# Performance work log

Hardware: AMD Instinct MI355X
Metric: run time of the kernel (lower is better)

The kernel has to match this reference:

```python
import jax, jax.numpy as jnp
import numpy as np

B, S, D, H, DFF = 4, 2048, 1024, 16, 4096
DK = D // H
EPS = 1e-9


def setup_inputs() -> dict:
    key = jax.random.key(0)
    ks = jax.random.split(key, 12)
    s = lambda k, shape, scale: jax.random.normal(k, shape, dtype=jnp.float32) * scale
    return {
        "x": s(ks[0], (B, S, D), 1.0),
        "mask": jnp.ones((B, 1, 1, S), dtype=jnp.int32),
        # Linear weights stored torch-style [out, in]
        "wq": s(ks[1], (D, D), D ** -0.5),
        "wk": s(ks[2], (D, D), D ** -0.5),
        "wv": s(ks[3], (D, D), D ** -0.5),
        "wo": s(ks[4], (D, D), D ** -0.5),
        "w1": s(ks[5], (DFF, D), D ** -0.5),
        "b1": jnp.zeros((DFF,), jnp.float32),
        "w2": s(ks[6], (D, DFF), DFF ** -0.5),
        "b2": jnp.zeros((D,), jnp.float32),
        "g1": jnp.ones((D,), jnp.float32),
        "be1": jnp.zeros((D,), jnp.float32),
        "g2": jnp.ones((D,), jnp.float32),
        "be2": jnp.zeros((D,), jnp.float32),
    }


def _layernorm(x, gamma, beta):
    # Matches AddAndNorm: torch.std uses Bessel correction (ddof=1)
    mean = jnp.mean(x, axis=-1, keepdims=True)
    var = jnp.sum((x - mean) ** 2, axis=-1, keepdims=True) / (x.shape[-1] - 1)
    return gamma * (x - mean) / jnp.sqrt(var + EPS) + beta


def _mha(x, mask, wq, wk, wv, wo):
    b, s, d = x.shape
    def proj(w):  # [b,s,d] @ [d,d]^T -> heads [b,h,s,dk]
        return (x @ w.T).reshape(b, s, H, DK).transpose(0, 2, 1, 3)
    q, k, v = proj(wq), proj(wk), proj(wv)
    scores = jnp.einsum("bhqd,bhkd->bhqk", q, k) / jnp.sqrt(jnp.float32(DK))
    scores = jnp.where(mask == 0, jnp.float32(-1e9), scores)
    attn = jax.nn.softmax(scores, axis=-1)
    out = jnp.einsum("bhqk,bhkd->bhqd", attn, v)
    out = out.transpose(0, 2, 1, 3).reshape(b, s, d)
    return out @ wo.T


def reference(x, mask, wq, wk, wv, wo, w1, b1, w2, b2, g1, be1, g2, be2):
    # Residual 1: x + MHA(LN(x))  (dropout = 0)
    h1 = x + _mha(_layernorm(x, g1, be1), mask, wq, wk, wv, wo)
    # Residual 2: h1 + FFN(LN(h1))
    z = _layernorm(h1, g2, be2)
    ffn = jax.nn.relu(z @ w1.T + b1) @ w2.T + b2
    return h1 + ffn
```

## Files before the change

kernel.cpp:

```cpp
#include <hip/hip_runtime.h>
#include <hip/hip_bf16.h>
#include <cstdint>
#include <cstddef>

typedef __attribute__((ext_vector_type(8))) short short8;
typedef __attribute__((ext_vector_type(4))) float floatx4;
typedef __attribute__((ext_vector_type(4))) unsigned short ushort4e;

#define B_   4
#define S_   2048
#define D_   1024
#define H_   16
#define DK_  64
#define DFF_ 4096
#define MTOT (B_ * S_)
#define QKVLD 3072

__device__ __forceinline__ float bf2f(unsigned short u) {
    union { unsigned int i; float f; } v; v.i = ((unsigned int)u) << 16; return v.f;
}
__device__ __forceinline__ unsigned short f2bf(float f) {
    union { float f; unsigned int i; } v; v.f = f;
    unsigned int u = v.i;
    u += 0x7fffu + ((u >> 16) & 1u);
    return (unsigned short)(u >> 16);
}
__device__ __forceinline__ void async_cp16(const void* g, void* l) {
    __builtin_amdgcn_global_load_lds(
        (const __attribute__((address_space(1))) unsigned int*)g,
        (__attribute__((address_space(3))) unsigned int*)l,
        16, 0, 0);
}

__global__ void dtype_probe(const unsigned short* __restrict__ x, int* flag) {
    __shared__ float red[4];
    const int tid = threadIdx.x;
    float mx = 0.f;
    #pragma unroll
    for (int i = 0; i < 16; i++) {
        float v = fabsf(bf2f(x[tid * 16 + i]));
        if (v != v) v = 1e30f;
        mx = fmaxf(mx, v);
    }
    #pragma unroll
    for (int off = 32; off > 0; off >>= 1) mx = fmaxf(mx, __shfl_down(mx, off));
    if ((tid & 63) == 0) red[tid >> 6] = mx;
    __syncthreads();
    if (tid == 0) {
        float m = fmaxf(fmaxf(red[0], red[1]), fmaxf(red[2], red[3]));
        *flag = (m > 50.f) ? 1 : 0;
    }
}

__device__ __forceinline__ void cvt8(const void* src, unsigned short* dst, int i, int fl) {
    if (fl) {
        const floatx4* s = (const floatx4*)src;
        floatx4 a = s[i * 2], b = s[i * 2 + 1];
        short8 o;
        o[0] = (short)f2bf(a[0]); o[1] = (short)f2bf(a[1]);
        o[2] = (short)f2bf(a[2]); o[3] = (short)f2bf(a[3]);
        o[4] = (short)f2bf(b[0]); o[5] = (short)f2bf(b[1]);
        o[6] = (short)f2bf(b[2]); o[7] = (short)f2bf(b[3]);
        ((short8*)dst)[i] = o;
    } else {
        ((short8*)dst)[i] = ((const short8*)src)[i];
    }
}

__global__ void cvt_kernel(const void* __restrict__ src,
                           unsigned short* __restrict__ dst,
                           int n8, const int* __restrict__ flag) {
    const int i = blockIdx.x * 256 + threadIdx.x;
    if (i >= n8) return;
    cvt8(src, dst, i, *flag);
}

__global__ void cvt4_kernel(const void* s0, const void* s1, const void* s2, const void* s3,
                            unsigned short* __restrict__ dst,
                            const int* __restrict__ flag) {
    const int t = blockIdx.x >> 9;
    const int i = (blockIdx.x & 511) * 256 + threadIdx.x;
    const void* s = (t == 0) ? s0 : (t == 1) ? s1 : (t == 2) ? s2 : s3;
    cvt8(s, dst + (size_t)t * (D_ * D_), i, *flag);
}

__global__ void cvt_small(const void* b1, const void* b2, const void* g1,
                          const void* be1, const void* g2, const void* be2,
                          unsigned short* db1, unsigned short* db2, unsigned short* dg1,
                          unsigned short* dbe1, unsigned short* dg2, unsigned short* dbe2,
                          const int* __restrict__ flag) {
    const int fl = *flag;
    for (int i = threadIdx.x; i < 1152; i += 256) {
        if (i < 512)       cvt8(b1,  db1,  i,        fl);
        else if (i < 640)  cvt8(b2,  db2,  i - 512,  fl);
        else if (i < 768)  cvt8(g1,  dg1,  i - 640,  fl);
        else if (i < 896)  cvt8(be1, dbe1, i - 768,  fl);
        else if (i < 1024) cvt8(g2,  dg2,  i - 896,  fl);
        else               cvt8(be2, dbe2, i - 1024, fl);
    }
}

#define BM 128
#define BN 128
#define BK 64

template<int RELU, int HAS_BIAS, int RES_MODE, int OUT_MODE>
__global__ __launch_bounds__(256)
void gemm_bt(const unsigned short* __restrict__ A, int lda,
             const unsigned short* __restrict__ W, int ldw,
             const unsigned short* __restrict__ bias,
             const void* resid,
             void* out,
             int M, int N, int K,
             const int* __restrict__ flagp)
{
    __shared__ unsigned short As[BM * BK];
    __shared__ unsigned short Bs[BN * BK];

    const int tid  = threadIdx.x;
    const int lane = tid & 63;
    const int wave = tid >> 6;
    const int wm = wave >> 1;
    const int wn = wave & 1;
    const int lr = lane & 15;
    const int lq = lane >> 4;

    const int m0 = blockIdx.y * BM;
    const int n0 = blockIdx.x * BN;

    int fl = 1;
    if (RES_MODE == 3 || OUT_MODE == 2) fl = *flagp;

    floatx4 acc[4][4];
    #pragma unroll
    for (int i = 0; i < 4; i++)
        #pragma unroll
        for (int j = 0; j < 4; j++)
            acc[i][j] = (floatx4){0.f, 0.f, 0.f, 0.f};

    const int lrow = lane >> 3;
    const int swz  = ((lane & 7) ^ lrow) * 8;
    const int rx   = lr & 7;
    const int p0   = ((lq)     ^ rx) * 8;
    const int p1   = ((4 + lq) ^ rx) * 8;

    for (int k0 = 0; k0 < K; k0 += BK) {
        #pragma unroll
        for (int t = 0; t < 4; t++) {
            const int row = wave * 32 + t * 8;
            async_cp16(A + (size_t)(m0 + row + lrow) * lda + k0 + swz, &As[row * BK]);
            async_cp16(W + (size_t)(n0 + row + lrow) * ldw + k0 + swz, &Bs[row * BK]);
        }
        __syncthreads();
        #pragma unroll
        for (int kk = 0; kk < 2; kk++) {
            const int pos = kk ? p1 : p0;
            short8 af[4], bfr[4];
            #pragma unroll
            for (int i = 0; i < 4; i++) {
                af[i]  = *(const short8*)(&As[(wm * 64 + i * 16 + lr) * BK + pos]);
                bfr[i] = *(const short8*)(&Bs[(wn * 64 + i * 16 + lr) * BK + pos]);
            }
            #pragma unroll
            for (int i = 0; i < 4; i++)
                #pragma unroll
                for (int j = 0; j < 4; j++)
                    acc[i][j] = __builtin_amdgcn_mfma_f32_16x16x32_bf16(
                                    af[i], bfr[j], acc[i][j], 0, 0, 0);
        }
        __syncthreads();
    }

    #pragma unroll
    for (int i = 0; i < 4; i++) {
        #pragma unroll
        for (int j = 0; j < 4; j++) {
            const int col = n0 + wn * 64 + j * 16 + lr;
            const float bv = HAS_BIAS ? bf2f(bias[col]) : 0.f;
            #pragma unroll
            for (int r = 0; r < 4; r++) {
                const int row = m0 + wm * 64 + i * 16 + lq * 4 + r;
                const size_t idx = (size_t)row * N + col;
                float vvv = acc[i][j][r] + bv;
                if (RES_MODE == 1) vvv += bf2f(((const unsigned short*)resid)[idx]);
                if (RES_MODE == 2) vvv += ((const float*)resid)[idx];
                if (RES_MODE == 3) vvv += fl ? ((const float*)resid)[idx]
                                             : bf2f(((const unsigned short*)resid)[idx]);
                if (RELU) vvv = fmaxf(vvv, 0.f);
                if (OUT_MODE == 1)      ((float*)out)[idx] = vvv;
                else if (OUT_MODE == 0) ((unsigned short*)out)[idx] = f2bf(vvv);
                else { if (fl) ((float*)out)[idx] = vvv;
                       else    ((unsigned short*)out)[idx] = f2bf(vvv); }
            }
        }
    }
}

#define GBM 256
#define GBN 256
#define GBK 64

__device__ __forceinline__ void gbar() {
    asm volatile("" ::: "memory");
    __builtin_amdgcn_s_barrier();
    asm volatile("" ::: "memory");
}

template<int RELU, int HAS_BIAS>
__global__ __launch_bounds__(512, 2)
void gemm256_bt(const unsigned short* __restrict__ A, int lda,
                const unsigned short* __restrict__ W, int ldw,
                const unsigned short* __restrict__ bias,
                unsigned short* __restrict__ out,
                int M, int N, int K)
{
    __shared__ unsigned short As[2][GBM * GBK];
    __shared__ unsigned short Bs[2][GBN * GBK];

    const int tid  = threadIdx.x;
    const int lane = tid & 63;
    const int wave = tid >> 6;
    const int wm   = wave >> 2;
    const int wn   = wave & 3;
    const int lr   = lane & 15;
    const int lq   = lane >> 4;

    const int m0 = blockIdx.y * GBM;
    const int n0 = blockIdx.x * GBN;

    const int lrow = lane >> 3;
    const int schk = ((lane & 7) ^ lrow) * 8;
    const int rx   = lr & 7;
    const int fp0  = ((lq)     ^ rx) * 8;
    const int fp1  = ((4 + lq) ^ rx) * 8;

    floatx4 acc[8][4];
    #pragma unroll
    for (int i = 0; i < 8; i++)
        #pragma unroll
        for (int j = 0; j < 4; j++)
            acc[i][j] = (floatx4){0.f, 0.f, 0.f, 0.f};

    const int nkt = K / GBK;

    #pragma unroll
    for (int g = 0; g < 4; g++) {
        async_cp16(A + (size_t)(m0 + g * 64 + wave * 8 + lrow) * lda + schk,
                   &As[0][g * 4096 + wave * 512]);
        async_cp16(W + (size_t)(n0 + g * 64 + wave * 8 + lrow) * ldw + schk,
                   &Bs[0][g * 4096 + wave * 512]);
    }
    asm volatile("s_waitcnt vmcnt(0)" ::: "memory");
    __syncthreads();

    for (int t = 0; t < nkt; ++t) {
        const int cur   = t & 1;
        const int knext = (t + 1) * GBK;
        const bool more = (t + 1 < nkt);
        short8 bfr[4][2];

        #pragma unroll
        for (int p = 0; p < 4; ++p) {
            short8 af[2][2];
            #pragma unroll
            for (int ii = 0; ii < 2; ii++)
                #pragma unroll
                for (int kk = 0; kk < 2; kk++)
                    af[ii][kk] = *(const short8*)
                        &As[cur][(wm * 128 + p * 32 + ii * 16 + lr) * GBK + (kk ? fp1 : fp0)];
            if (p == 0) {
                #pragma unroll
                for (int j = 0; j < 4; j++)
                    #pragma unroll
                    for (int kk = 0; kk < 2; kk++)
                        bfr[j][kk] = *(const short8*)
                            &Bs[cur][(wn * 64 + j * 16 + lr) * GBK + (kk ? fp1 : fp0)];
                if (more) {
                    #pragma unroll
                    for (int g = 0; g < 4; g++)
                        async_cp16(A + (size_t)(m0 + g * 64 + wave * 8 + lrow) * lda + knext + schk,
                                   &As[cur ^ 1][g * 4096 + wave * 512]);
                }
            }
            if (p == 1 && more) {
                #pragma unroll
                for (int g = 0; g < 4; g++)
                    async_cp16(W + (size_t)(n0 + g * 64 + wave * 8 + lrow) * ldw + knext + schk,
                               &Bs[cur ^ 1][g * 4096 + wave * 512]);
            }
            if (p == 3) asm volatile("s_waitcnt vmcnt(0)" ::: "memory");
            gbar();
            __builtin_amdgcn_s_setprio(1);
            #pragma unroll
            for (int kk = 0; kk < 2; kk++)
                #pragma unroll
                for (int ii = 0; ii < 2; ii++)
                    #pragma unroll
                    for (int j = 0; j < 4; j++)
                        acc[p * 2 + ii][j] = __builtin_amdgcn_mfma_f32_16x16x32_bf16(
                                                 af[ii][kk], bfr[j][kk],
                                                 acc[p * 2 + ii][j], 0, 0, 0);
            __builtin_amdgcn_s_setprio(0);
            gbar();
        }
    }

    #pragma unroll
    for (int i = 0; i < 8; i++) {
        #pragma unroll
        for (int j = 0; j < 4; j++) {
            const int col = n0 + wn * 64 + j * 16 + lr;
            const float bv = HAS_BIAS ? bf2f(bias[col]) : 0.f;
            #pragma unroll
            for (int r = 0; r < 4; r++) {
                const int row = m0 + wm * 128 + i * 16 + lq * 4 + r;
                float vvv = acc[i][j][r] + bv;
                if (RELU) vvv = fmaxf(vvv, 0.f);
                out[(size_t)row * N + col] = f2bf(vvv);
            }
        }
    }
}

template<int IN_MODE>
__global__ __launch_bounds__(256)
void ln_kernel(const void* __restrict__ Xv,
               const unsigned short* __restrict__ g,
               const unsigned short* __restrict__ be,
               unsigned short* __restrict__ out,
               const int* __restrict__ flagp)
{
    const int row = blockIdx.x;
    const int tid = threadIdx.x;
    int fl = 1;
    if (IN_MODE == 2) fl = *flagp;
    float x4[4];
    if (IN_MODE == 1 || fl) {
        const float* X = (const float*)Xv + (size_t)row * D_ + tid * 4;
        floatx4 t = *(const floatx4*)X;
        x4[0] = t[0]; x4[1] = t[1]; x4[2] = t[2]; x4[3] = t[3];
    } else {
        const unsigned short* X = (const unsigned short*)Xv + (size_t)row * D_ + tid * 4;
        ushort4e u = *(const ushort4e*)X;
        #pragma unroll
        for (int i = 0; i < 4; i++) x4[i] = bf2f(u[i]);
    }
    float s1 = x4[0] + x4[1] + x4[2] + x4[3];
    float s2 = x4[0]*x4[0] + x4[1]*x4[1] + x4[2]*x4[2] + x4[3]*x4[3];
    #pragma unroll
    for (int off = 32; off > 0; off >>= 1) {
        s1 += __shfl_down(s1, off);
        s2 += __shfl_down(s2, off);
    }
    __shared__ float r1[4], r2[4];
    const int wv = tid >> 6;
    if ((tid & 63) == 0) { r1[wv] = s1; r2[wv] = s2; }
    __syncthreads();
    s1 = r1[0] + r1[1] + r1[2] + r1[3];
    s2 = r2[0] + r2[1] + r2[2] + r2[3];
    const float mean = s1 * (1.0f / D_);
    const float var  = (s2 - (float)D_ * mean * mean) * (1.0f / (D_ - 1));
    const float rstd = rsqrtf(var + 1e-9f);

    ushort4e o4;
    #pragma unroll
    for (int i = 0; i < 4; i++) {
        const float gv = bf2f(g[tid * 4 + i]);
        const float bv = bf2f(be[tid * 4 + i]);
        o4[i] = f2bf(gv * (x4[i] - mean) * rstd + bv);
    }
    *(ushort4e*)(out + (size_t)row * D_ + tid * 4) = o4;
}

__global__ __launch_bounds__(256)
void vtrans(const unsigned short* __restrict__ V, int ldv,
            unsigned short* __restrict__ Vt)
{
    __shared__ unsigned short t[64 * 72];
    const int tid = threadIdx.x;
    const int kt  = blockIdx.x * 64;
    const int bh  = blockIdx.y;
    const int b   = bh >> 4, h = bh & 15;
    const int r   = tid >> 2;
    const int c4  = (tid & 3) * 16;
    const unsigned short* vp = V + (size_t)(b * S_ + kt + r) * ldv + h * DK_ + c4;
    *(short8*)&t[r * 72 + c4]     = *(const short8*)vp;
    *(short8*)&t[r * 72 + c4 + 8] = *(const short8*)(vp + 8);
    __syncthreads();
    short8 o0, o1;
    #pragma unroll
    for (int e = 0; e < 8; e++) {
        o0[e] = (short)t[(c4 + e) * 72 + r];
        o1[e] = (short)t[(c4 + 8 + e) * 72 + r];
    }
    unsigned short* op = Vt + ((size_t)bh * DK_ + r) * S_ + kt + c4;
    *(short8*)op       = o0;
    *(short8*)(op + 8) = o1;
}

#define ATK   64
#define KS_LD 64
#define PS_LD 72
#define NT_   (S_ / ATK)

__global__ __launch_bounds__(256)
void attn_mfma(const unsigned short* __restrict__ QKV,
               const unsigned short* __restrict__ Vt,
               const int* __restrict__ mask,
               unsigned short* __restrict__ ctx)
{
    __shared__ unsigned short Ks[ATK * KS_LD];
    __shared__ unsigned short Vts[DK_ * KS_LD];
    __shared__ unsigned short Ps[4][32 * PS_LD];
    __shared__ float maskadd[ATK];
    __shared__ float ared[4][32];

    const int tid  = threadIdx.x;
    const int lane = tid & 63;
    const int w    = tid >> 6;
    const int c    = lane & 15;
    const int qd   = lane >> 4;

    const int flat    = blockIdx.y * gridDim.x + blockIdx.x;
    const int logical = (flat & 7) * 128 + (flat >> 3);
    const int bh   = logical >> 4;
    const int b    = bh >> 4;
    const int h    = bh & 15;
    const int q0   = (logical & 15) * 128 + w * 32;

    const int lrow = lane >> 3;
    const int swz  = ((lane & 7) ^ lrow) * 8;
    const int cx   = c & 7;

    const float QS = 0.18033688f;
    short8 qf[2][2];
    #pragma unroll
    for (int jq = 0; jq < 2; jq++)
        #pragma unroll
        for (int kk = 0; kk < 2; kk++) {
            const unsigned short* qp =
                QKV + (size_t)(b * S_ + q0 + jq * 16 + c) * QKVLD + h * DK_ + kk * 32 + qd * 8;
            short8 t = *(const short8*)qp;
            short8 o;
            #pragma unroll
            for (int e = 0; e < 8; e++)
                o[e] = (short)f2bf(bf2f((unsigned short)t[e]) * QS);
            qf[jq][kk] = o;
        }

    floatx4 acc_o[2][4];
    #pragma unroll
    for (int iq = 0; iq < 2; iq++)
        #pragma unroll
        for (int jd = 0; jd < 4; jd++)
            acc_o[iq][jd] = (floatx4){0.f, 0.f, 0.f, 0.f};
    float lrun[2] = {0.f, 0.f};

    for (int kt = 0; kt < S_; kt += ATK) {
        {
            const unsigned short* kbase =
                QKV + 1024 + (size_t)(b * S_ + kt + w * 16) * QKVLD + h * DK_;
            const unsigned short* vbase =
                Vt + ((size_t)bh * DK_ + w * 16) * S_ + kt;
            #pragma unroll
            for (int t = 0; t < 2; t++) {
                async_cp16(kbase + (size_t)(t * 8 + lrow) * QKVLD + swz,
                           &Ks[(w * 16 + t * 8) * KS_LD]);
                async_cp16(vbase + (size_t)(t * 8 + lrow) * S_ + swz,
                           &Vts[(w * 16 + t * 8) * KS_LD]);
            }
            if (tid < ATK) maskadd[tid] = (mask[b * S_ + kt + tid] == 0) ? -1e9f : 0.f;
        }
        __syncthreads();

        floatx4 acc_s[4][2];
        #pragma unroll
        for (int i = 0; i < 4; i++)
            #pragma unroll
            for (int jq = 0; jq < 2; jq++)
                acc_s[i][jq] = (floatx4){0.f, 0.f, 0.f, 0.f};
        #pragma unroll
        for (int kk = 0; kk < 2; kk++) {
            const int pos = ((kk * 4 + qd) ^ cx) * 8;
            short8 kf[4];
            #pragma unroll
            for (int i = 0; i < 4; i++)
                kf[i] = *(const short8*)&Ks[(i * 16 + c) * KS_LD + pos];
            __builtin_amdgcn_s_setprio(1);
            #pragma unroll
            for (int i = 0; i < 4; i++)
                #pragma unroll
                for (int jq = 0; jq < 2; jq++)
                    acc_s[i][jq] = __builtin_amdgcn_mfma_f32_16x16x32_bf16(
                                       kf[i], qf[jq][kk], acc_s[i][jq], 0, 0, 0);
            __builtin_amdgcn_s_setprio(0);
        }

        floatx4 madd[4];
        #pragma unroll
        for (int i = 0; i < 4; i++)
            madd[i] = *(const floatx4*)&maskadd[i * 16 + qd * 4];

        #pragma unroll
        for (int jq = 0; jq < 2; jq++) {
            float ps = 0.f;
            #pragma unroll
            for (int i = 0; i < 4; i++) {
                floatx4 p;
                #pragma unroll
                for (int r = 0; r < 4; r++) {
                    p[r] = __builtin_amdgcn_exp2f(acc_s[i][jq][r] + madd[i][r]);
                    ps += p[r];
                }
                unsigned int w0, w1;
                asm("v_cvt_pk_bf16_f32 %0, %1, %2" : "=v"(w0) : "v"(p[0]), "v"(p[1]));
                asm("v_cvt_pk_bf16_f32 %0, %1, %2" : "=v"(w1) : "v"(p[2]), "v"(p[3]));
                uint2 pk; pk.x = w0; pk.y = w1;
                *(uint2*)&Ps[w][(jq * 16 + c) * PS_LD + i * 16 + qd * 4] = pk;
            }
            ps += __shfl_xor(ps, 16);
            ps += __shfl_xor(ps, 32);
            lrun[jq] += ps;
        }

        #pragma unroll
        for (int kk = 0; kk < 2; kk++) {
            const int pos = ((kk * 4 + qd) ^ cx) * 8;
            short8 pf[2], vf[4];
            #pragma unroll
            for (int iq = 0; iq < 2; iq++)
                pf[iq] = *(const short8*)&Ps[w][(iq * 16 + c) * PS_LD + kk * 32 + qd * 8];
            #pragma unroll
            for (int jd = 0; jd < 4; jd++)
                vf[jd] = *(const short8*)&Vts[(jd * 16 + c) * KS_LD + pos];
            __builtin_amdgcn_s_setprio(1);
            #pragma unroll
            for (int iq = 0; iq < 2; iq++)
                #pragma unroll
                for (int jd = 0; jd < 4; jd++)
                    acc_o[iq][jd] = __builtin_amdgcn_mfma_f32_16x16x32_bf16(
                                        pf[iq], vf[jd], acc_o[iq][jd], 0, 0, 0);
            __builtin_amdgcn_s_setprio(0);
        }
        __syncthreads();
    }

    if (lane < 16) { ared[w][c] = 1.f / lrun[0]; ared[w][16 + c] = 1.f / lrun[1]; }
    floatx4 lv0 = *(const floatx4*)&ared[w][qd * 4];
    floatx4 lv1 = *(const floatx4*)&ared[w][16 + qd * 4];
    #pragma unroll
    for (int iq = 0; iq < 2; iq++)
        #pragma unroll
        for (int jd = 0; jd < 4; jd++)
            #pragma unroll
            for (int r = 0; r < 4; r++) {
                const int row = q0 + iq * 16 + qd * 4 + r;
                const int col = h * DK_ + jd * 16 + c;
                const float inv = (iq == 0) ? lv0[r] : lv1[r];
                ctx[(size_t)(b * S_ + row) * D_ + col] = f2bf(acc_o[iq][jd][r] * inv);
            }
}

extern "C" void kernel_launch(void* const* d_in, const int* in_sizes, int n_in,
                              void* d_out, int out_size, void* d_ws, size_t ws_size,
                              hipStream_t stream)
{
    const void* x_raw  = d_in[0];
    const int*  mask   = (const int*)d_in[1];
    const void* wq_raw = d_in[2];
    const void* wk_raw = d_in[3];
    const void* wv_raw = d_in[4];
    const void* wo_raw = d_in[5];
    const void* w1_raw = d_in[6];
    const void* b1_raw = d_in[7];
    const void* w2_raw = d_in[8];
    const void* b2_raw = d_in[9];
    const void* g1_raw = d_in[10];
    const void* be1_raw= d_in[11];
    const void* g2_raw = d_in[12];
    const void* be2_raw= d_in[13];

    char* ws = (char*)d_ws;
    const size_t MB = 1024 * 1024;
    int* flag = (int*)ws;
    unsigned short* cb1  = (unsigned short*)(ws + 1 * 1024);
    unsigned short* cb2  = (unsigned short*)(ws + 16 * 1024);
    unsigned short* cg1  = (unsigned short*)(ws + 32 * 1024);
    unsigned short* cbe1 = (unsigned short*)(ws + 40 * 1024);
    unsigned short* cg2  = (unsigned short*)(ws + 48 * 1024);
    unsigned short* cbe2 = (unsigned short*)(ws + 56 * 1024);
    unsigned short* cwqkvo = (unsigned short*)(ws + 1 * MB);
    unsigned short* cwqkv  = cwqkvo;
    unsigned short* cwo    = cwqkvo + 3 * (D_ * D_);
    unsigned short* cw1  = (unsigned short*)(ws + 9 * MB);
    unsigned short* cw2  = (unsigned short*)(ws + 17 * MB);
    unsigned short* xn1  = (unsigned short*)(ws + 25 * MB);
    unsigned short* ctx  = (unsigned short*)(ws + 25 * MB);
    unsigned short* zbuf = (unsigned short*)(ws + 25 * MB);
    unsigned short* qkv  = (unsigned short*)(ws + 41 * MB);
    float*          h1   = (float*)(ws + 57 * MB);
    unsigned short* vt   = (unsigned short*)d_out;
    unsigned short* xn2  = (unsigned short*)d_out;

    dtype_probe<<<1, 256, 0, stream>>>((const unsigned short*)x_raw, flag);
    cvt_small<<<1, 256, 0, stream>>>(b1_raw, b2_raw, g1_raw, be1_raw, g2_raw, be2_raw,
                                     cb1, cb2, cg1, cbe1, cg2, cbe2, flag);
    cvt4_kernel<<<2048, 256, 0, stream>>>(wq_raw, wk_raw, wv_raw, wo_raw, cwqkvo, flag);
    cvt_kernel<<<(DFF_ * D_ / 8 + 255) / 256, 256, 0, stream>>>(w1_raw, cw1, DFF_ * D_ / 8, flag);
    cvt_kernel<<<(D_ * DFF_ / 8 + 255) / 256, 256, 0, stream>>>(w2_raw, cw2, D_ * DFF_ / 8, flag);

    const dim3 blk(256);
    const dim3 blk5(512);
    const dim3 gs(D_ / BN, MTOT / BM);
    const dim3 gq256(QKVLD / GBN, MTOT / GBM);
    const dim3 gf256(2048 / GBN, MTOT / GBM);

    ln_kernel<2><<<MTOT, blk, 0, stream>>>(x_raw, cg1, cbe1, xn1, flag);
    gemm256_bt<0,0><<<gq256, blk5, 0, stream>>>(xn1, D_, cwqkv, D_, nullptr, qkv, MTOT, QKVLD, D_);
    vtrans<<<dim3(S_ / 64, B_ * H_), blk, 0, stream>>>(qkv + 2048, QKVLD, vt);
    attn_mfma<<<dim3(S_ / 128, B_ * H_), blk, 0, stream>>>(qkv, vt, mask, ctx);
    gemm_bt<0,0,3,1><<<gs, blk, 0, stream>>>(ctx, D_, cwo, D_, nullptr, x_raw, h1, MTOT, D_, D_, flag);
    ln_kernel<1><<<MTOT, blk, 0, stream>>>(h1, cg2, cbe2, xn2, flag);
    gemm256_bt<1,1><<<gf256, blk5, 0, stream>>>(xn2, D_, cw1, D_, cb1, zbuf, MTOT, 2048, D_);
    gemm_bt<0,0,2,1><<<gs, blk, 0, stream>>>(zbuf, 2048, cw2, DFF_, nullptr, h1, h1, MTOT, D_, 2048, flag);
    const unsigned short* w1c = cw1 + (size_t)2048 * D_;
    gemm256_bt<1,1><<<gf256, blk5, 0, stream>>>(xn2, D_, w1c, D_, cb1 + 2048, zbuf, MTOT, 2048, D_);
    gemm_bt<0,1,2,2><<<gs, blk, 0, stream>>>(zbuf, 2048, cw2 + 2048, DFF_, cb2, h1, d_out, MTOT, D_, 2048, flag);
}
```

Before: 569.6 us.

## Double attention query rows per block and add XCD-aware tile remapping to GEMMs

```diff
diff --git a/kernel.cpp b/kernel.cpp
--- a/kernel.cpp
+++ b/kernel.cpp
@@ -125,8 +125,11 @@
     const int lr = lane & 15;
     const int lq = lane >> 4;
 
-    const int m0 = blockIdx.y * BM;
-    const int n0 = blockIdx.x * BN;
+    const int nwg     = gridDim.x * gridDim.y;
+    const int flat    = blockIdx.y * gridDim.x + blockIdx.x;
+    const int logical = (flat & 7) * (nwg >> 3) + (flat >> 3);
+    const int m0 = (logical / gridDim.x) * BM;
+    const int n0 = (logical % gridDim.x) * BN;
 
     int fl = 1;
     if (RES_MODE == 3 || OUT_MODE == 2) fl = *flagp;
@@ -225,8 +228,11 @@
     const int lr   = lane & 15;
     const int lq   = lane >> 4;
 
-    const int m0 = blockIdx.y * GBM;
-    const int n0 = blockIdx.x * GBN;
+    const int nwg     = gridDim.x * gridDim.y;
+    const int flat    = blockIdx.y * gridDim.x + blockIdx.x;
+    const int logical = (flat & 7) * (nwg >> 3) + (flat >> 3);
+    const int m0 = (logical / gridDim.x) * GBM;
+    const int n0 = (logical % gridDim.x) * GBN;
 
     const int lrow = lane >> 3;
     const int schk = ((lane & 7) ^ lrow) * 8;
@@ -413,7 +419,7 @@
     __shared__ unsigned short Vts[DK_ * KS_LD];
     __shared__ unsigned short Ps[4][32 * PS_LD];
     __shared__ float maskadd[ATK];
-    __shared__ float ared[4][32];
+    __shared__ float ared[4][64];
 
     const int tid  = threadIdx.x;
     const int lane = tid & 63;
@@ -422,39 +428,44 @@
     const int qd   = lane >> 4;
 
     const int flat    = blockIdx.y * gridDim.x + blockIdx.x;
-    const int logical = (flat & 7) * 128 + (flat >> 3);
-    const int bh   = logical >> 4;
+    const int logical = (flat & 7) * 64 + (flat >> 3);
+    const int bh   = logical >> 3;
     const int b    = bh >> 4;
     const int h    = bh & 15;
-    const int q0   = (logical & 15) * 128 + w * 32;
+    const int qb   = (logical & 7) * 256 + w * 32;
 
     const int lrow = lane >> 3;
     const int swz  = ((lane & 7) ^ lrow) * 8;
     const int cx   = c & 7;
 
     const float QS = 0.18033688f;
-    short8 qf[2][2];
-    #pragma unroll
-    for (int jq = 0; jq < 2; jq++)
-        #pragma unroll
-        for (int kk = 0; kk < 2; kk++) {
-            const unsigned short* qp =
-                QKV + (size_t)(b * S_ + q0 + jq * 16 + c) * QKVLD + h * DK_ + kk * 32 + qd * 8;
-            short8 t = *(const short8*)qp;
-            short8 o;
-            #pragma unroll
-            for (int e = 0; e < 8; e++)
-                o[e] = (short)f2bf(bf2f((unsigned short)t[e]) * QS);
-            qf[jq][kk] = o;
-        }
-
-    floatx4 acc_o[2][4];
-    #pragma unroll
-    for (int iq = 0; iq < 2; iq++)
-        #pragma unroll
-        for (int jd = 0; jd < 4; jd++)
-            acc_o[iq][jd] = (floatx4){0.f, 0.f, 0.f, 0.f};
-    float lrun[2] = {0.f, 0.f};
+    short8 qf[2][2][2];
+    #pragma unroll
+    for (int qh = 0; qh < 2; qh++)
+        #pragma unroll
+        for (int jq = 0; jq < 2; jq++)
+            #pragma unroll
+            for (int kk = 0; kk < 2; kk++) {
+                const unsigned short* qp =
+                    QKV + (size_t)(b * S_ + qb + qh * 128 + jq * 16 + c) * QKVLD
+                        + h * DK_ + kk * 32 + qd * 8;
+                short8 t = *(const short8*)qp;
+                short8 o;
+                #pragma unroll
+                for (int e = 0; e < 8; e++)
+                    o[e] = (short)f2bf(bf2f((unsigned short)t[e]) * QS);
+                qf[qh][jq][kk] = o;
+            }
+
+    floatx4 acc_o[2][2][4];
+    #pragma unroll
+    for (int qh = 0; qh < 2; qh++)
+        #pragma unroll
+        for (int iq = 0; iq < 2; iq++)
+            #pragma unroll
+            for (int jd = 0; jd < 4; jd++)
+                acc_o[qh][iq][jd] = (floatx4){0.f, 0.f, 0.f, 0.f};
+    float lrun[2][2] = {{0.f, 0.f}, {0.f, 0.f}};
 
     for (int kt = 0; kt < S_; kt += ATK) {
         {
@@ -473,92 +484,106 @@
         }
         __syncthreads();
 
-        floatx4 acc_s[4][2];
-        #pragma unroll
-        for (int i = 0; i < 4; i++)
-            #pragma unroll
-            for (int jq = 0; jq < 2; jq++)
-                acc_s[i][jq] = (floatx4){0.f, 0.f, 0.f, 0.f};
-        #pragma unroll
-        for (int kk = 0; kk < 2; kk++) {
-            const int pos = ((kk * 4 + qd) ^ cx) * 8;
-            short8 kf[4];
+        #pragma unroll
+        for (int qh = 0; qh < 2; qh++) {
+            floatx4 acc_s[4][2];
             #pragma unroll
             for (int i = 0; i < 4; i++)
-                kf[i] = *(const short8*)&Ks[(i * 16 + c) * KS_LD + pos];
-            __builtin_amdgcn_s_setprio(1);
+                #pragma unroll
+                for (int jq = 0; jq < 2; jq++)
+                    acc_s[i][jq] = (floatx4){0.f, 0.f, 0.f, 0.f};
+            #pragma unroll
+            for (int kk = 0; kk < 2; kk++) {
+                const int pos = ((kk * 4 + qd) ^ cx) * 8;
+                short8 kf[4];
+                #pragma unroll
+                for (int i = 0; i < 4; i++)
+                    kf[i] = *(const short8*)&Ks[(i * 16 + c) * KS_LD + pos];
+                __builtin_amdgcn_s_setprio(1);
+                #pragma unroll
+                for (int i = 0; i < 4; i++)
+                    #pragma unroll
+                    for (int jq = 0; jq < 2; jq++)
+                        acc_s[i][jq] = __builtin_amdgcn_mfma_f32_16x16x32_bf16(
+                                           kf[i], qf[qh][jq][kk], acc_s[i][jq], 0, 0, 0);
+                __builtin_amdgcn_s_setprio(0);
+            }
+
+            floatx4 madd[4];
             #pragma unroll
             for (int i = 0; i < 4; i++)
-                #pragma unroll
-                for (int jq = 0; jq < 2; jq++)
-                    acc_s[i][jq] = __builtin_amdgcn_mfma_f32_16x16x32_bf16(
-                                       kf[i], qf[jq][kk], acc_s[i][jq], 0, 0, 0);
-            __builtin_amdgcn_s_setprio(0);
-        }
-
-        floatx4 madd[4];
-        #pragma unroll
-        for (int i = 0; i < 4; i++)
-            madd[i] = *(const floatx4*)&maskadd[i * 16 + qd * 4];
-
-        #pragma unroll
-        for (int jq = 0; jq < 2; jq++) {
-            float ps = 0.f;
-            #pragma unroll
-            for (int i = 0; i < 4; i++) {
-                floatx4 p;
-                #pragma unroll
-                for (int r = 0; r < 4; r++) {
-                    p[r] = __builtin_amdgcn_exp2f(acc_s[i][jq][r] + madd[i][r]);
-                    ps += p[r];
+                madd[i] = *(const floatx4*)&maskadd[i * 16 + qd * 4];
+
+            #pragma unroll
+            for (int jq = 0; jq < 2; jq++) {
+                float ps = 0.f;
+                #pragma unroll
+                for (int i = 0; i < 4; i++) {
+                    floatx4 p;
+                    #pragma unroll
+                    for (int r = 0; r < 4; r++) {
+                        p[r] = __builtin_amdgcn_exp2f(acc_s[i][jq][r] + madd[i][r]);
+                        ps += p[r];
+                    }
+                    unsigned int w0, w1;
+                    asm("v_cvt_pk_bf16_f32 %0, %1, %2" : "=v"(w0) : "v"(p[0]), "v"(p[1]));
+                    asm("v_cvt_pk_bf16_f32 %0, %1, %2" : "=v"(w1) : "v"(p[2]), "v"(p[3]));
+                    uint2 pk; pk.x = w0; pk.y = w1;
+                    *(uint2*)&Ps[w][(jq * 16 + c) * PS_LD + i * 16 + qd * 4] = pk;
                 }
-                unsigned int w0, w1;
-                asm("v_cvt_pk_bf16_f32 %0, %1, %2" : "=v"(w0) : "v"(p[0]), "v"(p[1]));
-                asm("v_cvt_pk_bf16_f32 %0, %1, %2" : "=v"(w1) : "v"(p[2]), "v"(p[3]));
-                uint2 pk; pk.x = w0; pk.y = w1;
-                *(uint2*)&Ps[w][(jq * 16 + c) * PS_LD + i * 16 + qd * 4] = pk;
-            }
-            ps += __shfl_xor(ps, 16);
-            ps += __shfl_xor(ps, 32);
-            lrun[jq] += ps;
-        }
-
-        #pragma unroll
-        for (int kk = 0; kk < 2; kk++) {
-            const int pos = ((kk * 4 + qd) ^ cx) * 8;
-            short8 pf[2], vf[4];
-            #pragma unroll
-            for (int iq = 0; iq < 2; iq++)
-                pf[iq] = *(const short8*)&Ps[w][(iq * 16 + c) * PS_LD + kk * 32 + qd * 8];
-            #pragma unroll
-            for (int jd = 0; jd < 4; jd++)
-                vf[jd] = *(const short8*)&Vts[(jd * 16 + c) * KS_LD + pos];
-            __builtin_amdgcn_s_setprio(1);
-            #pragma unroll
-            for (int iq = 0; iq < 2; iq++)
+                ps += __shfl_xor(ps, 16);
+                ps += __shfl_xor(ps, 32);
+                lrun[qh][jq] += ps;
+            }
+
+            #pragma unroll
+            for (int kk = 0; kk < 2; kk++) {
+                const int pos = ((kk * 4 + qd) ^ cx) * 8;
+                short8 pf[2], vf[4];
+                #pragma unroll
+                for (int iq = 0; iq < 2; iq++)
+                    pf[iq] = *(const short8*)&Ps[w][(iq * 16 + c) * PS_LD + kk * 32 + qd * 8];
                 #pragma unroll
                 for (int jd = 0; jd < 4; jd++)
-                    acc_o[iq][jd] = __builtin_amdgcn_mfma_f32_16x16x32_bf16(
-                                        pf[iq], vf[jd], acc_o[iq][jd], 0, 0, 0);
-            __builtin_amdgcn_s_setprio(0);
+                    vf[jd] = *(const short8*)&Vts[(jd * 16 + c) * KS_LD + pos];
+                __builtin_amdgcn_s_setprio(1);
+                #pragma unroll
+                for (int iq = 0; iq < 2; iq++)
+                    #pragma unroll
+                    for (int jd = 0; jd < 4; jd++)
+                        acc_o[qh][iq][jd] = __builtin_amdgcn_mfma_f32_16x16x32_bf16(
+                                                pf[iq], vf[jd], acc_o[qh][iq][jd], 0, 0, 0);
+                __builtin_amdgcn_s_setprio(0);
+            }
         }
         __syncthreads();
     }
 
-    if (lane < 16) { ared[w][c] = 1.f / lrun[0]; ared[w][16 + c] = 1.f / lrun[1]; }
-    floatx4 lv0 = *(const floatx4*)&ared[w][qd * 4];
-    floatx4 lv1 = *(const floatx4*)&ared[w][16 + qd * 4];
-    #pragma unroll
-    for (int iq = 0; iq < 2; iq++)
-        #pragma unroll
-        for (int jd = 0; jd < 4; jd++)
-            #pragma unroll
-            for (int r = 0; r < 4; r++) {
-                const int row = q0 + iq * 16 + qd * 4 + r;
-                const int col = h * DK_ + jd * 16 + c;
-                const float inv = (iq == 0) ? lv0[r] : lv1[r];
-                ctx[(size_t)(b * S_ + row) * D_ + col] = f2bf(acc_o[iq][jd][r] * inv);
-            }
+    if (lane < 16) {
+        ared[w][c]      = 1.f / lrun[0][0];
+        ared[w][16 + c] = 1.f / lrun[0][1];
+        ared[w][32 + c] = 1.f / lrun[1][0];
+        ared[w][48 + c] = 1.f / lrun[1][1];
+    }
+    floatx4 lv[2][2];
+    #pragma unroll
+    for (int qh = 0; qh < 2; qh++)
+        #pragma unroll
+        for (int iq = 0; iq < 2; iq++)
+            lv[qh][iq] = *(const floatx4*)&ared[w][qh * 32 + iq * 16 + qd * 4];
+    #pragma unroll
+    for (int qh = 0; qh < 2; qh++)
+        #pragma unroll
+        for (int iq = 0; iq < 2; iq++)
+            #pragma unroll
+            for (int jd = 0; jd < 4; jd++)
+                #pragma unroll
+                for (int r = 0; r < 4; r++) {
+                    const int row = qb + qh * 128 + iq * 16 + qd * 4 + r;
+                    const int col = h * DK_ + jd * 16 + c;
+                    ctx[(size_t)(b * S_ + row) * D_ + col] =
+                        f2bf(acc_o[qh][iq][jd][r] * lv[qh][iq][r]);
+                }
 }
 
 extern "C" void kernel_launch(void* const* d_in, const int* in_sizes, int n_in,
@@ -618,7 +643,7 @@
     ln_kernel<2><<<MTOT, blk, 0, stream>>>(x_raw, cg1, cbe1, xn1, flag);
     gemm256_bt<0,0><<<gq256, blk5, 0, stream>>>(xn1, D_, cwqkv, D_, nullptr, qkv, MTOT, QKVLD, D_);
     vtrans<<<dim3(S_ / 64, B_ * H_), blk, 0, stream>>>(qkv + 2048, QKVLD, vt);
-    attn_mfma<<<dim3(S_ / 128, B_ * H_), blk, 0, stream>>>(qkv, vt, mask, ctx);
+    attn_mfma<<<dim3(S_ / 256, B_ * H_), blk, 0, stream>>>(qkv, vt, mask, ctx);
     gemm_bt<0,0,3,1><<<gs, blk, 0, stream>>>(ctx, D_, cwo, D_, nullptr, x_raw, h1, MTOT, D_, D_, flag);
     ln_kernel<1><<<MTOT, blk, 0, stream>>>(h1, cg2, cbe2, xn2, flag);
     gemm256_bt<1,1><<<gf256, blk5, 0, stream>>>(xn2, D_, cw1, D_, cb1, zbuf, MTOT, 2048, D_);
```

After: 561.3 us. Within noise of the previous version (-1.5%).
